# Performance work log

Measured on AMD Instinct MI355X. Metric: run time of the kernel, lower is better.

Reference implementation:

```python
import jax, jax.numpy as jnp
import numpy as np

TEMPERATURE = 0.5
EPS = 1e-12  # torch F.normalize eps


def _l2_normalize(x, eps=EPS):
    n = jnp.linalg.norm(x, axis=1, keepdims=True)
    return x / jnp.maximum(n, eps)


def setup_inputs() -> dict:
    key = jax.random.key(0)
    k1, k2 = jax.random.split(key)
    B, D = 4096, 512
    return {
        "polyline_embs": jax.random.normal(k1, (B, D), dtype=jnp.float32),
        "c_embs": jax.random.normal(k2, (B, D), dtype=jnp.float32),
    }


def reference(polyline_embs, c_embs):
    b = polyline_embs.shape[0]
    # double-normalization in the original (F.normalize then cosine_similarity)
    # is idempotent on unit vectors, so sim = Z @ Z^T with Z unit-normalized.
    z = _l2_normalize(jnp.concatenate([polyline_embs, c_embs], axis=0))  # [2B, D]
    sim = z @ z.T  # [2B, 2B] cosine similarity
    # positives: diag offsets +B and -B
    idx = jnp.arange(b)
    sim_ij = sim[idx, idx + b]
    sim_ji = sim[idx + b, idx]
    positives = jnp.concatenate([sim_ij, sim_ji], axis=0)  # [2B]
    nominator = jnp.exp(positives / TEMPERATURE)
    mask = 1.0 - jnp.eye(2 * b, dtype=sim.dtype)
    denominator = jnp.sum(mask * jnp.exp(sim / TEMPERATURE), axis=1)  # [2B]
    all_losses = -jnp.log(nominator / denominator)
    return jnp.sum(all_losses) / (2 * b)
```

## Files before the change

### kernel.cpp

```cpp
#include <hip/hip_runtime.h>
#include <hip/hip_bf16.h>

#define B_ROWS 4096
#define D_DIM  512
#define N_ROWS 8192
#define BM 128
#define BN 128
#define BKB 128
#define NBLK (N_ROWS / BM)
#define NPAIR (NBLK * (NBLK + 1) / 2)

typedef float f32x4 __attribute__((ext_vector_type(4)));

__global__ __launch_bounds__(256) void prep_kernel(
    const float* __restrict__ poly, const float* __restrict__ cemb,
    unsigned char* __restrict__ Z, float* __restrict__ row_sum,
    float* __restrict__ pos, unsigned int* __restrict__ counter)
{
    const int r = blockIdx.x;
    const int t = threadIdx.x;
    const float* prow = poly + (size_t)r * D_DIM;
    const float* crow = cemb + (size_t)r * D_DIM;

    const float2 pv = *(const float2*)(prow + 2 * t);
    const float2 cv = *(const float2*)(crow + 2 * t);

    float ssp = pv.x * pv.x + pv.y * pv.y;
    float ssc = cv.x * cv.x + cv.y * cv.y;
    float dt  = pv.x * cv.x + pv.y * cv.y;

    #pragma unroll
    for (int m = 1; m < 64; m <<= 1) {
        ssp += __shfl_xor(ssp, m);
        ssc += __shfl_xor(ssc, m);
        dt  += __shfl_xor(dt,  m);
    }
    __shared__ float red[3][4];
    const int wave = t >> 6;
    if ((t & 63) == 0) { red[0][wave] = ssp; red[1][wave] = ssc; red[2][wave] = dt; }
    __syncthreads();
    ssp = red[0][0] + red[0][1] + red[0][2] + red[0][3];
    ssc = red[1][0] + red[1][1] + red[1][2] + red[1][3];
    dt  = red[2][0] + red[2][1] + red[2][2] + red[2][3];

    const float sp = 1.0f / fmaxf(sqrtf(ssp), 1e-12f);
    const float sc = 1.0f / fmaxf(sqrtf(ssc), 1e-12f);

    unsigned char* zp = Z + (size_t)r * D_DIM;
    unsigned char* zc = Z + (size_t)(r + B_ROWS) * D_DIM;
    const int pk = __builtin_amdgcn_cvt_pk_fp8_f32(pv.x * sp, pv.y * sp, 0, false);
    const int ck = __builtin_amdgcn_cvt_pk_fp8_f32(cv.x * sc, cv.y * sc, 0, false);
    *(unsigned short*)(zp + 2 * t) = (unsigned short)(pk & 0xffff);
    *(unsigned short*)(zc + 2 * t) = (unsigned short)(ck & 0xffff);

    if (t == 0) {
        pos[r] = dt * sp * sc;
        row_sum[2 * r]     = 0.0f;
        row_sum[2 * r + 1] = 0.0f;
        if (r == 0) *counter = 0u;
    }
}

__global__ __launch_bounds__(256) void sim_kernel(
    const unsigned char* __restrict__ Z, float* __restrict__ row_sum,
    const float* __restrict__ pos, float* __restrict__ out,
    unsigned int* __restrict__ counter)
{
    __shared__ __align__(16) unsigned char As[BM * BKB];
    __shared__ __align__(16) unsigned char Bs[BN * BKB];
    __shared__ float rAcc[BM];
    __shared__ float cAcc[BN];
    __shared__ unsigned int lastFlag;

    const int t0 = blockIdx.x;
    int bi = (int)((129.0f - sqrtf(16641.0f - 8.0f * (float)t0)) * 0.5f);
    #define CFN(b) ((b) * (129 - (b)) / 2)
    while (CFN(bi + 1) <= t0) ++bi;
    while (CFN(bi) > t0) --bi;
    const int bj = bi + (t0 - CFN(bi));
    #undef CFN
    const bool diag = (bi == bj);

    const int ibase = bi * BM;
    const int jbase = bj * BN;
    const int tid   = threadIdx.x;

    const int srow = tid >> 3;
    const int gchk = (tid & 7) ^ (srow & 7);

    const int wave = tid >> 6;
    const int lane = tid & 63;
    const int wi = (wave >> 1) * 64;
    const int wj = (wave & 1) * 64;
    const int quad = lane >> 4;
    const int c    = lane & 15;

    f32x4 acc[4][4] = {};

    for (int k0 = 0; k0 < D_DIM; k0 += BKB) {
        #pragma unroll
        for (int it = 0; it < 4; ++it) {
            const int row = it * 32 + srow;
            const unsigned char* ga = Z + (size_t)(ibase + row) * D_DIM + k0 + gchk * 16;
            __builtin_amdgcn_global_load_lds(
                (const __attribute__((address_space(1))) void*)ga,
                (__attribute__((address_space(3))) void*)(As + it * 4096 + tid * 16),
                16, 0, 0);
        }
        if (!diag) {
            #pragma unroll
            for (int it = 0; it < 4; ++it) {
                const int row = it * 32 + srow;
                const unsigned char* gb = Z + (size_t)(jbase + row) * D_DIM + k0 + gchk * 16;
                __builtin_amdgcn_global_load_lds(
                    (const __attribute__((address_space(1))) void*)gb,
                    (__attribute__((address_space(3))) void*)(Bs + it * 4096 + tid * 16),
                    16, 0, 0);
            }
        }
        __syncthreads();

        const unsigned char* bsrc = diag ? As : Bs;
        #pragma unroll
        for (int kk = 0; kk < BKB; kk += 32) {
            const int sw  = ((kk >> 4) + (quad >> 1)) ^ (c & 7);
            const int sub = (quad & 1) * 8;
            long a[4], b[4];
            #pragma unroll
            for (int ti = 0; ti < 4; ++ti)
                a[ti] = *(const long*)&As[(wi + ti * 16 + c) * BKB + sw * 16 + sub];
            #pragma unroll
            for (int tj = 0; tj < 4; ++tj)
                b[tj] = *(const long*)&bsrc[(wj + tj * 16 + c) * BKB + sw * 16 + sub];
            #pragma unroll
            for (int ti = 0; ti < 4; ++ti)
                #pragma unroll
                for (int tj = 0; tj < 4; ++tj)
                    acc[ti][tj] = __builtin_amdgcn_mfma_f32_16x16x32_fp8_fp8(
                        a[ti], b[tj], acc[ti][tj], 0, 0, 0);
        }
        __syncthreads();
    }

    if (tid < BM) { rAcc[tid] = 0.0f; cAcc[tid] = 0.0f; }
    __syncthreads();

    const float K2 = 2.885390081777927f;
    float col[4] = {0.0f, 0.0f, 0.0f, 0.0f};
    #pragma unroll
    for (int ti = 0; ti < 4; ++ti) {
        const int li = wi + ti * 16 + quad * 4;
        #pragma unroll
        for (int r = 0; r < 4; ++r) {
            const int gi = ibase + li + r;
            float v = 0.0f;
            #pragma unroll
            for (int tj = 0; tj < 4; ++tj) {
                const int gj = jbase + wj + tj * 16 + c;
                const float e = (gj > gi) ? exp2f(K2 * acc[ti][tj][r]) : 0.0f;
                v += e;
                col[tj] += e;
            }
            v += __shfl_xor(v, 1);
            v += __shfl_xor(v, 2);
            v += __shfl_xor(v, 4);
            v += __shfl_xor(v, 8);
            if (c == 0)
                atomicAdd(&rAcc[li + r], v);
        }
    }
    #pragma unroll
    for (int tj = 0; tj < 4; ++tj) {
        float w = col[tj];
        w += __shfl_xor(w, 16);
        w += __shfl_xor(w, 32);
        if (quad == 0)
            atomicAdd(&cAcc[wj + tj * 16 + c], w);
    }
    __syncthreads();

    if (tid < BM)
        atomicAdd(&row_sum[ibase + tid], rAcc[tid]);
    else
        atomicAdd(&row_sum[jbase + tid - BM], cAcc[tid - BM]);

    __syncthreads();
    if (tid == 0) {
        unsigned int old = __hip_atomic_fetch_add(
            counter, 1u, __ATOMIC_RELAXED, __HIP_MEMORY_SCOPE_AGENT);
        lastFlag = (old == NPAIR - 1) ? 1u : 0u;
    }
    __syncthreads();
    if (lastFlag) {
        float accL = 0.0f, accP = 0.0f;
        for (int i = tid; i < N_ROWS; i += 256) {
            const float rs = __hip_atomic_load(
                &row_sum[i], __ATOMIC_RELAXED, __HIP_MEMORY_SCOPE_AGENT);
            accL += __logf(rs);
        }
        for (int r = tid; r < B_ROWS; r += 256)
            accP += pos[r];
        #pragma unroll
        for (int m = 1; m < 64; m <<= 1) {
            accL += __shfl_xor(accL, m);
            accP += __shfl_xor(accP, m);
        }
        if (lane == 0) { rAcc[wave] = accL; cAcc[wave] = accP; }
        __syncthreads();
        if (tid == 0) {
            float L = 0.0f, P = 0.0f;
            #pragma unroll
            for (int w = 0; w < 4; ++w) { L += rAcc[w]; P += cAcc[w]; }
            out[0] = (L - 4.0f * P) / (float)N_ROWS;
        }
    }
}

extern "C" void kernel_launch(void* const* d_in, const int* in_sizes, int n_in,
                              void* d_out, int out_size, void* d_ws, size_t ws_size,
                              hipStream_t stream) {
    const float* poly = (const float*)d_in[0];
    const float* cemb = (const float*)d_in[1];

    unsigned char* Z       = (unsigned char*)d_ws;
    float*         row_sum = (float*)((char*)d_ws + (size_t)N_ROWS * D_DIM);
    float*         pos     = row_sum + N_ROWS;
    unsigned int*  counter = (unsigned int*)(pos + B_ROWS);
    float*         out     = (float*)d_out;

    prep_kernel<<<B_ROWS, 256, 0, stream>>>(poly, cemb, Z, row_sum, pos, counter);
    sim_kernel<<<NPAIR, 256, 0, stream>>>(Z, row_sum, pos, out, counter);
}
```

Before: 131.6 us.

## Double-buffer LDS tiles and switch to 16x16x128 scaled fp8 MFMA

Makes the A/B shared-memory tiles double-buffered so the async global-to-LDS load of the next K slice is issued before computing on the current one, dropping one barrier per iteration. Replaces four 16x16x32 fp8 MFMAs per K slice with a single gfx950 scaled 16x16x128 f8f6f4 MFMA using unit scales (0x7f). Fragments are now loaded as two 16-byte LDS reads per tile. This doubles LDS use, which may lower occupancy. The staged loads for the next buffer are issued right before compute with no wait specific to them, so the final barrier is relied on for ordering.

```diff
diff --git a/kernel.cpp b/kernel.cpp
--- a/kernel.cpp
+++ b/kernel.cpp
@@ -11,6 +11,8 @@
 #define NPAIR (NBLK * (NBLK + 1) / 2)
 
 typedef float f32x4 __attribute__((ext_vector_type(4)));
+typedef int   v4i   __attribute__((ext_vector_type(4)));
+typedef int   v8i   __attribute__((ext_vector_type(8)));
 
 __global__ __launch_bounds__(256) void prep_kernel(
     const float* __restrict__ poly, const float* __restrict__ cemb,
@@ -66,8 +68,8 @@
     const float* __restrict__ pos, float* __restrict__ out,
     unsigned int* __restrict__ counter)
 {
-    __shared__ __align__(16) unsigned char As[BM * BKB];
-    __shared__ __align__(16) unsigned char Bs[BN * BKB];
+    __shared__ __align__(16) unsigned char As[2][BM * BKB];
+    __shared__ __align__(16) unsigned char Bs[2][BN * BKB];
     __shared__ float rAcc[BM];
     __shared__ float cAcc[BN];
     __shared__ unsigned int lastFlag;
@@ -97,14 +99,17 @@
 
     f32x4 acc[4][4] = {};
 
-    for (int k0 = 0; k0 < D_DIM; k0 += BKB) {
+    const int sg0 = (((quad << 1)    ) ^ (c & 7)) * 16;
+    const int sg1 = (((quad << 1) | 1) ^ (c & 7)) * 16;
+
+    auto stage = [&](int buf, int k0) {
         #pragma unroll
         for (int it = 0; it < 4; ++it) {
             const int row = it * 32 + srow;
             const unsigned char* ga = Z + (size_t)(ibase + row) * D_DIM + k0 + gchk * 16;
             __builtin_amdgcn_global_load_lds(
                 (const __attribute__((address_space(1))) void*)ga,
-                (__attribute__((address_space(3))) void*)(As + it * 4096 + tid * 16),
+                (__attribute__((address_space(3))) void*)(&As[buf][it * 4096 + tid * 16]),
                 16, 0, 0);
         }
         if (!diag) {
@@ -114,30 +119,43 @@
                 const unsigned char* gb = Z + (size_t)(jbase + row) * D_DIM + k0 + gchk * 16;
                 __builtin_amdgcn_global_load_lds(
                     (const __attribute__((address_space(1))) void*)gb,
-                    (__attribute__((address_space(3))) void*)(Bs + it * 4096 + tid * 16),
+                    (__attribute__((address_space(3))) void*)(&Bs[buf][it * 4096 + tid * 16]),
                     16, 0, 0);
             }
         }
-        __syncthreads();
-
-        const unsigned char* bsrc = diag ? As : Bs;
-        #pragma unroll
-        for (int kk = 0; kk < BKB; kk += 32) {
-            const int sw  = ((kk >> 4) + (quad >> 1)) ^ (c & 7);
-            const int sub = (quad & 1) * 8;
-            long a[4], b[4];
-            #pragma unroll
-            for (int ti = 0; ti < 4; ++ti)
-                a[ti] = *(const long*)&As[(wi + ti * 16 + c) * BKB + sw * 16 + sub];
+    };
+
+    stage(0, 0);
+    __syncthreads();
+
+    #pragma unroll
+    for (int t = 0; t < 4; ++t) {
+        if (t < 3) stage((t + 1) & 1, (t + 1) * BKB);
+
+        const unsigned char* ab = As[t & 1];
+        const unsigned char* bb = diag ? As[t & 1] : Bs[t & 1];
+
+        v8i bfr[4];
+        #pragma unroll
+        for (int tj = 0; tj < 4; ++tj) {
+            const unsigned char* base = bb + (wj + tj * 16 + c) * BKB;
+            const v4i lo = *(const v4i*)(base + sg0);
+            const v4i hi = *(const v4i*)(base + sg1);
+            bfr[tj] = __builtin_shufflevector(lo, hi, 0, 1, 2, 3, 4, 5, 6, 7);
+        }
+        #pragma unroll
+        for (int ti = 0; ti < 4; ++ti) {
+            const unsigned char* base = ab + (wi + ti * 16 + c) * BKB;
+            const v4i lo = *(const v4i*)(base + sg0);
+            const v4i hi = *(const v4i*)(base + sg1);
+            const v8i afr = __builtin_shufflevector(lo, hi, 0, 1, 2, 3, 4, 5, 6, 7);
             #pragma unroll
             for (int tj = 0; tj < 4; ++tj)
-                b[tj] = *(const long*)&bsrc[(wj + tj * 16 + c) * BKB + sw * 16 + sub];
-            #pragma unroll
-            for (int ti = 0; ti < 4; ++ti)
-                #pragma unroll
-                for (int tj = 0; tj < 4; ++tj)
-                    acc[ti][tj] = __builtin_amdgcn_mfma_f32_16x16x32_fp8_fp8(
-                        a[ti], b[tj], acc[ti][tj], 0, 0, 0);
+                acc[ti][tj] = __builtin_amdgcn_mfma_scale_f32_16x16x128_f8f6f4(
+                    afr, bfr[tj], acc[ti][tj],
+                    0, 0,
+                    0, 0x7f7f7f7f,
+                    0, 0x7f7f7f7f);
         }
         __syncthreads();
     }
```

Result: slower. 156.7 us (+19.1%).
